# Performance work log

Hardware: AMD Instinct MI355X
Metric: run time of the kernel (lower is better)

The kernel has to match this reference:

```python
import jax, jax.numpy as jnp
import numpy as np

N = 100_000        # nodes
E = 1_600_000      # edges (avg in-degree 16)
D_IN = 128
D_OUT = 128
K = 2              # hops


def setup_inputs() -> dict:
    key = jax.random.key(0)
    k1, k2, k3, k4 = jax.random.split(key, 4)
    feat = jax.random.normal(k1, (N, D_IN), dtype=jnp.float32)
    src = jax.random.randint(k2, (E,), 0, N, dtype=jnp.int64)
    # guarantee every node has in-degree >= 1 so deg**-0.5 is finite
    # (first N dst entries cover all nodes, rest random)
    dst_rand = jax.random.randint(k3, (E - N,), 0, N, dtype=jnp.int64)
    dst = jnp.concatenate([jnp.arange(N, dtype=jnp.int64), dst_rand])
    # xavier-normal-ish linear params: Linear(D_IN*(K+1) -> D_OUT)
    fan_in = D_IN * (K + 1)
    std = np.sqrt(2.0) * np.sqrt(2.0 / (fan_in + D_OUT))  # gain('relu') * xavier
    W = jax.random.normal(k4, (D_OUT, fan_in), dtype=jnp.float32) * std
    b = jnp.zeros((D_OUT,), dtype=jnp.float32)
    return {"feat": feat, "src": src, "dst": dst, "W": W, "b": b}


def reference(feat, src, dst, W, b):
    n = feat.shape[0]
    # in-degree based symmetric normalization: D^{-1/2} A D^{-1/2}
    deg = jax.ops.segment_sum(jnp.ones_like(dst, dtype=feat.dtype), dst,
                              num_segments=n)
    norm = (deg ** -0.5)[:, None]                 # [N, 1]
    fstack = [feat]
    h = feat
    for _ in range(K):
        h = h * norm                              # pre-scale by D^{-1/2}
        # SpMM: sum of source features into destination nodes
        h = jax.ops.segment_sum(h[src], dst, num_segments=n)
        h = h * norm                              # post-scale by D^{-1/2}
        fstack.append(h)
    x = jnp.concatenate(fstack, axis=-1)          # [N, D_IN*(K+1)]
    return x @ W.T + b
```

## Files before the change

kernel.cpp:

```cpp
#include <hip/hip_runtime.h>
#include <hip/hip_bf16.h>


#define D 128
#define TPB 256
#define GEMM_GRID 768

#define BSH 9
#define BSZ 512
#define NBMAX 256
#define EPT 16
#define CH (TPB * EPT)
#define LCAP 16384

typedef __attribute__((ext_vector_type(8))) short short8;
typedef __attribute__((ext_vector_type(4))) float f32x4;

__device__ __forceinline__ ushort f2bf(float f) {
    unsigned u = __float_as_uint(f);
    u += 0x7fff + ((u >> 16) & 1);
    return (ushort)(u >> 16);
}
__device__ __forceinline__ unsigned pack2bf(float x, float y) {
    return (unsigned)f2bf(x) | ((unsigned)f2bf(y) << 16);
}
__device__ __forceinline__ float bf_lo(unsigned v) { return __uint_as_float(v << 16); }
__device__ __forceinline__ float bf_hi(unsigned v) { return __uint_as_float(v & 0xffff0000u); }

__global__ __launch_bounds__(TPB) void mega_kernel(
    const int* __restrict__ src, const int* __restrict__ dst,
    int* __restrict__ gCursor, unsigned* __restrict__ tmp,
    const float* __restrict__ feat, unsigned* __restrict__ featb,
    const float* __restrict__ W, ushort* __restrict__ Wb,
    int e, int n, int nbin, int npre) {
    __shared__ int hist[NBMAX];
    __shared__ int cellBase[NBMAX];
    int t = threadIdx.x;
    int bid = blockIdx.x;

    if (bid < nbin) {
        hist[t] = 0;
        __syncthreads();
        int base = bid * CH;
        int b[EPT]; unsigned pk[EPT]; int r[EPT];
#pragma unroll
        for (int k = 0; k < EPT; ++k) {
            int i = base + k * TPB + t;
            b[k] = -1;
            if (i < e) {
                int d = dst[i];
                b[k] = d >> BSH;
                pk[k] = ((unsigned)src[i] << BSH) | (unsigned)(d & (BSZ - 1));
                r[k] = atomicAdd(&hist[b[k]], 1);
            }
        }
        __syncthreads();
        int h = hist[t];
        cellBase[t] = h ? t * LCAP + atomicAdd(&gCursor[t], h) : 0;
        __syncthreads();
#pragma unroll
        for (int k = 0; k < EPT; ++k)
            if (b[k] >= 0) tmp[cellBase[b[k]] + r[k]] = pk[k];
    } else if (bid < nbin + npre) {
        int gid = (bid - nbin) * TPB + t;
        int node = gid >> 6, c = gid & 63;
        if (node >= n) return;
        float2 f = ((const float2*)(feat + (size_t)node * D))[c];
        featb[(size_t)node * 64 + c] = pack2bf(f.x, f.y);
    } else {
        int i = ((bid - nbin - npre) * TPB + t) * 4;
        float4 w = *(const float4*)(W + i);
        ushort4 o;
        o.x = f2bf(w.x); o.y = f2bf(w.y); o.z = f2bf(w.z); o.w = f2bf(w.w);
        *(ushort4*)(Wb + i) = o;
    }
}

__global__ __launch_bounds__(TPB) void bucket_csr_kernel(
    const unsigned* __restrict__ tmp, const int* __restrict__ gCursor,
    int2* __restrict__ rsdeg, float* __restrict__ norm, int* __restrict__ csr,
    int n) {
    __shared__ int cnt[BSZ];
    __shared__ int off[BSZ];
    __shared__ int pr[TPB];
    __shared__ int lcsr[LCAP];
    int t = threadIdx.x;
    int bkt = blockIdx.x;
    int beg = bkt * LCAP;
    int m = gCursor[bkt];
    int end = beg + m;
    cnt[t] = 0; cnt[t + TPB] = 0;
    __syncthreads();
    for (int i = beg + t; i < end; i += TPB)
        atomicAdd(&cnt[tmp[i] & (BSZ - 1)], 1);
    __syncthreads();
    int c0 = cnt[2 * t], c1 = cnt[2 * t + 1];
    int own = c0 + c1;
    pr[t] = own;
    __syncthreads();
    for (int o = 1; o < TPB; o <<= 1) {
        int x = (t >= o) ? pr[t - o] : 0;
        __syncthreads();
        pr[t] += x;
        __syncthreads();
    }
    int ex = pr[t] - own;
    off[2 * t] = ex;
    off[2 * t + 1] = ex + c0;
    __syncthreads();
    cnt[t] = 0; cnt[t + TPB] = 0;
    __syncthreads();
    for (int i = beg + t; i < end; i += TPB) {
        unsigned v = tmp[i];
        int l = v & (BSZ - 1);
        int r = atomicAdd(&cnt[l], 1);
        int idx = off[l] + r;
        if (idx < LCAP) lcsr[idx] = (int)(v >> BSH);
    }
    __syncthreads();
    int mm = m < LCAP ? m : LCAP;
    for (int i = t; i < mm; i += TPB) csr[beg + i] = lcsr[i];
    int node0 = bkt << BSH;
    for (int l = t; l < BSZ; l += TPB) {
        int node = node0 + l;
        if (node < n) {
            rsdeg[node] = make_int2(beg + off[l], cnt[l]);
            norm[node] = rsqrtf((float)cnt[l]);
        }
    }
}

__global__ __launch_bounds__(TPB) void spmm_kernel(
    const uint4* __restrict__ hin4, const int2* __restrict__ rsdeg,
    const int* __restrict__ csr, const float* __restrict__ norm,
    unsigned* __restrict__ hout, int n) {
    int w = (blockIdx.x * TPB + threadIdx.x) >> 6;
    if (w >= n) return;
    int lane = threadIdx.x & 63;
    int q = lane >> 4;
    int c = lane & 15;
    int2 rd = rsdeg[w];
    int beg = rd.x, end = rd.x + rd.y;
    float acc[8] = {};
#pragma unroll 4
    for (int j = beg + q; j < end; j += 4) {
        int u = csr[j];
        float s = norm[u];
        uint4 v = hin4[(u << 4) + c];
        acc[0] = fmaf(s, bf_lo(v.x), acc[0]);
        acc[1] = fmaf(s, bf_hi(v.x), acc[1]);
        acc[2] = fmaf(s, bf_lo(v.y), acc[2]);
        acc[3] = fmaf(s, bf_hi(v.y), acc[3]);
        acc[4] = fmaf(s, bf_lo(v.z), acc[4]);
        acc[5] = fmaf(s, bf_hi(v.z), acc[5]);
        acc[6] = fmaf(s, bf_lo(v.w), acc[6]);
        acc[7] = fmaf(s, bf_hi(v.w), acc[7]);
    }
#pragma unroll
    for (int k = 0; k < 8; ++k) {
        acc[k] += __shfl_xor(acc[k], 16, 64);
        acc[k] += __shfl_xor(acc[k], 32, 64);
    }
    if (q == 0) {
        float nv = norm[w];
        uint4 r;
        r.x = pack2bf(acc[0] * nv, acc[1] * nv);
        r.y = pack2bf(acc[2] * nv, acc[3] * nv);
        r.z = pack2bf(acc[4] * nv, acc[5] * nv);
        r.w = pack2bf(acc[6] * nv, acc[7] * nv);
        *(uint4*)(hout + (size_t)w * 64 + c * 4) = r;
    }
}

__global__ __launch_bounds__(TPB) void gemm_mfma_kernel(
    const ushort* __restrict__ featb, const ushort* __restrict__ h1b,
    const ushort* __restrict__ h2b, const ushort* __restrict__ Wb,
    const float* __restrict__ bias, float* __restrict__ out, int n, int ntiles) {
    int lane = threadIdx.x & 63;
    int wave = threadIdx.x >> 6;
    int m = lane & 15, q = lane >> 4;

    short8 b[12][2];
#pragma unroll
    for (int ks = 0; ks < 12; ++ks)
#pragma unroll
        for (int t = 0; t < 2; ++t)
            b[ks][t] = *(const short8*)(Wb + (size_t)(wave * 32 + t * 16 + m) * 384
                                        + ks * 32 + q * 8);
    float bv0 = bias[wave * 32 + m];
    float bv1 = bias[wave * 32 + 16 + m];

    const ushort* srcs[3] = {featb, h1b, h2b};

    for (int tile = blockIdx.x; tile < ntiles; tile += gridDim.x) {
        int row = tile * 16 + m;
        bool va = row < n;
        size_t arow = (size_t)row * D;
        short8 a[12] = {};
        if (va) {
#pragma unroll
            for (int ks = 0; ks < 12; ++ks)
                a[ks] = *(const short8*)(srcs[ks >> 2] + arow + (ks & 3) * 32 + q * 8);
        }
        f32x4 acc0 = {}, acc1 = {};
#pragma unroll
        for (int ks = 0; ks < 12; ++ks) {
            acc0 = __builtin_amdgcn_mfma_f32_16x16x32_bf16(a[ks], b[ks][0], acc0, 0, 0, 0);
            acc1 = __builtin_amdgcn_mfma_f32_16x16x32_bf16(a[ks], b[ks][1], acc1, 0, 0, 0);
        }
        int r0 = tile * 16 + q * 4;
#pragma unroll
        for (int r = 0; r < 4; ++r) {
            int rw = r0 + r;
            if (rw < n) {
                size_t o = (size_t)rw * D + wave * 32 + m;
                out[o] = acc0[r] + bv0;
                out[o + 16] = acc1[r] + bv1;
            }
        }
    }
}

extern "C" void kernel_launch(void* const* d_in, const int* in_sizes, int n_in,
                              void* d_out, int out_size, void* d_ws, size_t ws_size,
                              hipStream_t stream) {
    const float* feat = (const float*)d_in[0];
    const int* src    = (const int*)d_in[1];
    const int* dst    = (const int*)d_in[2];
    const float* W    = (const float*)d_in[3];
    const float* bias = (const float*)d_in[4];
    float* out        = (float*)d_out;

    const int N = in_sizes[0] / D;
    const int E = in_sizes[1];
    const int NB = (N + BSZ - 1) >> BSH;

    char* ws = (char*)d_ws;
    size_t off = 0;
    auto bump = [&](size_t bytes) {
        char* p = ws + off;
        off += (bytes + 255) & ~(size_t)255;
        return p;
    };
    int* gCursor     = (int*)bump((size_t)NBMAX * 4);
    float* norm      = (float*)bump((size_t)N * 4);
    int2* rsdeg      = (int2*)bump((size_t)N * 8);
    unsigned* tmp    = (unsigned*)bump((size_t)NB * LCAP * 4);
    int* csr         = (int*)bump((size_t)NB * LCAP * 4);
    unsigned* featb  = (unsigned*)bump((size_t)N * 64 * 4);
    unsigned* h1b    = (unsigned*)bump((size_t)N * 64 * 4);
    unsigned* h2b    = (unsigned*)bump((size_t)N * 64 * 4);
    ushort* Wb       = (ushort*)bump((size_t)D * 384 * 2);
    (void)ws_size;

    hipMemsetAsync(gCursor, 0, (size_t)NBMAX * 4, stream);

    const int nbin = (E + CH - 1) / CH;
    const int npre = (N * 64 + TPB - 1) / TPB;
    const int nwcv = (D * 384 / 4 + TPB - 1) / TPB;
    mega_kernel<<<nbin + npre + nwcv, TPB, 0, stream>>>(
        src, dst, gCursor, tmp, feat, featb, W, Wb, E, N, nbin, npre);

    bucket_csr_kernel<<<NB, TPB, 0, stream>>>(tmp, gCursor, rsdeg, norm, csr, N);

    const int spmm_blocks = (N * 64 + TPB - 1) / TPB;
    spmm_kernel<<<spmm_blocks, TPB, 0, stream>>>((const uint4*)featb, rsdeg, csr, norm, h1b, N);
    spmm_kernel<<<spmm_blocks, TPB, 0, stream>>>((const uint4*)h1b, rsdeg, csr, norm, h2b, N);

    const int ntiles = (N + 15) / 16;
    gemm_mfma_kernel<<<GEMM_GRID, TPB, 0, stream>>>(
        (const ushort*)featb, (const ushort*)h1b, (const ushort*)h2b,
        Wb, bias, out, N, ntiles);
}
```

Measured before the change: 308.8 us.

## Slice bf16 feature layout into 8 column slabs for cache-local SpMM gathers

Feature buffers are stored as 8 column slices of 16 bf16 values per node, and each SpMM block handles one slice of 4 destination nodes, so the gather working set per slice (about 3.2 MB) can stay resident in cache. The first SpMM also writes a copy pre-scaled by norm squared, which lets the second SpMM drop the per-neighbour norm load and multiply. The GEMM A-loads are re-indexed to read the sliced layout. In exchange the csr and rsdeg arrays are re-read once per slice, each gather is only 32 bytes, and one extra N×128 bf16 buffer is written.

```diff
diff --git a/kernel.cpp b/kernel.cpp
--- a/kernel.cpp
+++ b/kernel.cpp
@@ -65,8 +65,9 @@
         int gid = (bid - nbin) * TPB + t;
         int node = gid >> 6, c = gid & 63;
         if (node >= n) return;
-        float2 f = ((const float2*)(feat + (size_t)node * D))[c];
-        featb[(size_t)node * 64 + c] = pack2bf(f.x, f.y);
+        float2 f = ((const float2*)feat)[(size_t)node * 64 + c];
+        int sl = c >> 3, cc = c & 7;
+        featb[((size_t)sl * n + node) * 8 + cc] = pack2bf(f.x, f.y);
     } else {
         int i = ((bid - nbin - npre) * TPB + t) * 4;
         float4 w = *(const float4*)(W + i);
@@ -130,45 +131,69 @@
     }
 }
 
-__global__ __launch_bounds__(TPB) void spmm_kernel(
-    const uint4* __restrict__ hin4, const int2* __restrict__ rsdeg,
+__global__ __launch_bounds__(TPB) void spmm1_kernel(
+    const unsigned* __restrict__ featb, const int2* __restrict__ rsdeg,
     const int* __restrict__ csr, const float* __restrict__ norm,
-    unsigned* __restrict__ hout, int n) {
-    int w = (blockIdx.x * TPB + threadIdx.x) >> 6;
-    if (w >= n) return;
-    int lane = threadIdx.x & 63;
-    int q = lane >> 4;
-    int c = lane & 15;
-    int2 rd = rsdeg[w];
+    unsigned* __restrict__ h1b, unsigned* __restrict__ h1p, int n) {
+    int wave = threadIdx.x >> 6, lane = threadIdx.x & 63;
+    int slice = blockIdx.x & 7;
+    int v = (blockIdx.x >> 3) * 4 + wave;
+    if (v >= n) return;
+    int e = lane >> 3, c = lane & 7;
+    int2 rd = rsdeg[v];
     int beg = rd.x, end = rd.x + rd.y;
-    float acc[8] = {};
-#pragma unroll 4
-    for (int j = beg + q; j < end; j += 4) {
+    const unsigned* hs = featb + (size_t)slice * n * 8;
+    float ax = 0.f, ay = 0.f;
+#pragma unroll 2
+    for (int j = beg + e; j < end; j += 8) {
         int u = csr[j];
         float s = norm[u];
-        uint4 v = hin4[(u << 4) + c];
-        acc[0] = fmaf(s, bf_lo(v.x), acc[0]);
-        acc[1] = fmaf(s, bf_hi(v.x), acc[1]);
-        acc[2] = fmaf(s, bf_lo(v.y), acc[2]);
-        acc[3] = fmaf(s, bf_hi(v.y), acc[3]);
-        acc[4] = fmaf(s, bf_lo(v.z), acc[4]);
-        acc[5] = fmaf(s, bf_hi(v.z), acc[5]);
-        acc[6] = fmaf(s, bf_lo(v.w), acc[6]);
-        acc[7] = fmaf(s, bf_hi(v.w), acc[7]);
-    }
-#pragma unroll
-    for (int k = 0; k < 8; ++k) {
-        acc[k] += __shfl_xor(acc[k], 16, 64);
-        acc[k] += __shfl_xor(acc[k], 32, 64);
-    }
-    if (q == 0) {
-        float nv = norm[w];
-        uint4 r;
-        r.x = pack2bf(acc[0] * nv, acc[1] * nv);
-        r.y = pack2bf(acc[2] * nv, acc[3] * nv);
-        r.z = pack2bf(acc[4] * nv, acc[5] * nv);
-        r.w = pack2bf(acc[6] * nv, acc[7] * nv);
-        *(uint4*)(hout + (size_t)w * 64 + c * 4) = r;
+        unsigned hv = hs[u * 8 + c];
+        ax = fmaf(s, bf_lo(hv), ax);
+        ay = fmaf(s, bf_hi(hv), ay);
+    }
+#pragma unroll
+    for (int o = 8; o < 64; o <<= 1) {
+        ax += __shfl_xor(ax, o, 64);
+        ay += __shfl_xor(ay, o, 64);
+    }
+    if (e == 0) {
+        float nv = norm[v];
+        size_t idx = ((size_t)slice * n + v) * 8 + c;
+        h1b[idx] = pack2bf(ax * nv, ay * nv);
+        float n2 = nv * nv;
+        h1p[idx] = pack2bf(ax * n2, ay * n2);
+    }
+}
+
+__global__ __launch_bounds__(TPB) void spmm2_kernel(
+    const unsigned* __restrict__ h1p, const int2* __restrict__ rsdeg,
+    const int* __restrict__ csr, const float* __restrict__ norm,
+    unsigned* __restrict__ h2b, int n) {
+    int wave = threadIdx.x >> 6, lane = threadIdx.x & 63;
+    int slice = blockIdx.x & 7;
+    int v = (blockIdx.x >> 3) * 4 + wave;
+    if (v >= n) return;
+    int e = lane >> 3, c = lane & 7;
+    int2 rd = rsdeg[v];
+    int beg = rd.x, end = rd.x + rd.y;
+    const unsigned* hs = h1p + (size_t)slice * n * 8;
+    float ax = 0.f, ay = 0.f;
+#pragma unroll 2
+    for (int j = beg + e; j < end; j += 8) {
+        int u = csr[j];
+        unsigned hv = hs[u * 8 + c];
+        ax += bf_lo(hv);
+        ay += bf_hi(hv);
+    }
+#pragma unroll
+    for (int o = 8; o < 64; o <<= 1) {
+        ax += __shfl_xor(ax, o, 64);
+        ay += __shfl_xor(ay, o, 64);
+    }
+    if (e == 0) {
+        float nv = norm[v];
+        h2b[((size_t)slice * n + v) * 8 + c] = pack2bf(ax * nv, ay * nv);
     }
 }
 
@@ -195,12 +220,15 @@
     for (int tile = blockIdx.x; tile < ntiles; tile += gridDim.x) {
         int row = tile * 16 + m;
         bool va = row < n;
-        size_t arow = (size_t)row * D;
         short8 a[12] = {};
         if (va) {
 #pragma unroll
-            for (int ks = 0; ks < 12; ++ks)
-                a[ks] = *(const short8*)(srcs[ks >> 2] + arow + (ks & 3) * 32 + q * 8);
+            for (int ks = 0; ks < 12; ++ks) {
+                int col0 = (ks & 3) * 32 + q * 8;
+                int sl = col0 >> 4, o = col0 & 15;
+                a[ks] = *(const short8*)(srcs[ks >> 2]
+                                         + ((size_t)sl * n + row) * 16 + o);
+            }
         }
         f32x4 acc0 = {}, acc1 = {};
 #pragma unroll
@@ -249,6 +277,7 @@
     int* csr         = (int*)bump((size_t)NB * LCAP * 4);
     unsigned* featb  = (unsigned*)bump((size_t)N * 64 * 4);
     unsigned* h1b    = (unsigned*)bump((size_t)N * 64 * 4);
+    unsigned* h1p    = (unsigned*)bump((size_t)N * 64 * 4);
     unsigned* h2b    = (unsigned*)bump((size_t)N * 64 * 4);
     ushort* Wb       = (ushort*)bump((size_t)D * 384 * 2);
     (void)ws_size;
@@ -263,9 +292,9 @@
 
     bucket_csr_kernel<<<NB, TPB, 0, stream>>>(tmp, gCursor, rsdeg, norm, csr, N);
 
-    const int spmm_blocks = (N * 64 + TPB - 1) / TPB;
-    spmm_kernel<<<spmm_blocks, TPB, 0, stream>>>((const uint4*)featb, rsdeg, csr, norm, h1b, N);
-    spmm_kernel<<<spmm_blocks, TPB, 0, stream>>>((const uint4*)h1b, rsdeg, csr, norm, h2b, N);
+    const int nsp = ((N + 3) / 4) * 8;
+    spmm1_kernel<<<nsp, TPB, 0, stream>>>(featb, rsdeg, csr, norm, h1b, h1p, N);
+    spmm2_kernel<<<nsp, TPB, 0, stream>>>(h1p, rsdeg, csr, norm, h2b, N);
 
     const int ntiles = (N + 15) / 16;
     gemm_mfma_kernel<<<GEMM_GRID, TPB, 0, stream>>>(
```

After: 606.7 us. +96.5%, slower.
